# Optimization experiments

Measured on AMD Instinct MI355X. Metric: run time of the kernel, lower is better.

The kernel has to match this reference:

```python
import jax, jax.numpy as jnp
import numpy as np

MEMORY_SIZE = 2000
SHAPE = (512, 8, 8)
D = int(np.prod(SHAPE))  # 32768
LAM = 0.0005  # hard-shrink threshold (1/memory_size convention)
EPS = 1e-12   # F.normalize eps


def _l2_normalize(x, axis):
    # matches F.normalize(p=2): x / max(||x||, eps)
    n = jnp.sqrt(jnp.sum(x * x, axis=axis, keepdims=True))
    return x / jnp.maximum(n, EPS)


def _hard_shrink(x):
    return jnp.where(jnp.abs(x) > LAM, x, jnp.zeros_like(x))


def setup_inputs() -> dict:
    key = jax.random.key(0)
    k1, k2 = jax.random.split(key)
    feature = jax.random.normal(k1, (256, *SHAPE), dtype=jnp.float32)
    memory = jax.random.normal(k2, (MEMORY_SIZE, D), dtype=jnp.float32)
    return {"feature": feature, "memory": memory}


def reference(feature, memory):
    B = feature.shape[0]
    flat = feature.reshape(B, -1)                     # [B, D]
    fn = _l2_normalize(flat, axis=1)                  # [B, D]
    mn = _l2_normalize(memory, axis=1)                # [M, D]
    w = jnp.einsum('bd,md->bm', fn, mn)               # cosine similarity [B, M]
    w = jax.nn.softmax(w, axis=1)
    w = _hard_shrink(w)
    w = jax.nn.softmax(w, axis=1)
    mem_feat = jnp.einsum('bm,md->bd', w, memory)     # [B, D]
    mem_feat = mem_feat.reshape(B, *SHAPE)
    return (mem_feat, w)
```

## Files before the change

### kernel.cpp

```cpp
#include <hip/hip_runtime.h>
#include <math.h>


#define D_DIM 32768
#define B_DIM 256
#define M_DIM 2000
#define M_PAD 2048
#define NS1 16
#define KSLAB (D_DIM / NS1)
#define LAM 0.0005f
#define LDB 72

typedef __attribute__((ext_vector_type(8))) short bf16x8;
typedef __attribute__((ext_vector_type(4))) float f32x4;

#define GLOBAL_AS __attribute__((address_space(1)))
#define LDS_AS __attribute__((address_space(3)))

__device__ __forceinline__ void cp_async16(const void* g, void* l) {
  __builtin_amdgcn_global_load_lds((const GLOBAL_AS unsigned int*)g,
                                   (LDS_AS unsigned int*)l, 16, 0, 0);
}

__device__ __forceinline__ unsigned short f2bf(float f) {
  union { float f; unsigned u; } v; v.f = f;
  unsigned r = v.u + 0x7FFFu + ((v.u >> 16) & 1u);
  return (unsigned short)(r >> 16);
}

__global__ __launch_bounds__(256) void zero_kernel(float* __restrict__ p, int n) {
  int i = blockIdx.x * 256 + threadIdx.x;
  if (i < n) p[i] = 0.f;
}

__global__ __launch_bounds__(256) void prep_feat_kernel(const float* __restrict__ src,
                                                        unsigned short* __restrict__ dst,
                                                        float* __restrict__ rn_inv) {
  const size_t row = blockIdx.x;
  const int t = threadIdx.x;
  const float4* p = (const float4*)(src + row * (size_t)D_DIM);
  ushort4* q = (ushort4*)(dst + row * (size_t)D_DIM);
  float s = 0.f;
  for (int i = t; i < D_DIM / 4; i += 256) {
    float4 v = p[i];
    s = fmaf(v.x, v.x, s); s = fmaf(v.y, v.y, s);
    s = fmaf(v.z, v.z, s); s = fmaf(v.w, v.w, s);
    ushort4 b; b.x = f2bf(v.x); b.y = f2bf(v.y); b.z = f2bf(v.z); b.w = f2bf(v.w);
    q[i] = b;
  }
  #pragma unroll
  for (int off = 32; off > 0; off >>= 1) s += __shfl_down(s, off, 64);
  __shared__ float partial[4];
  if ((t & 63) == 0) partial[t >> 6] = s;
  __syncthreads();
  if (t == 0) {
    float tt = partial[0] + partial[1] + partial[2] + partial[3];
    rn_inv[row] = 1.0f / fmaxf(sqrtf(tt), 1e-12f);
  }
}

__global__ __launch_bounds__(256) void gemm1_fused(const unsigned short* __restrict__ F16,
                                                   const float* __restrict__ mem,
                                                   unsigned short* __restrict__ Mem16,
                                                   float* __restrict__ Spart,
                                                   float* __restrict__ rnm_sq) {
  __shared__ __align__(16) unsigned short Asm[256 * 64];
  __shared__ __align__(16) unsigned short Bsm[64 * LDB];
  const int t = threadIdx.x;
  const int m0 = blockIdx.x * 64;
  const int kbase = blockIdx.y * KSLAB;
  const int wid = t >> 6, lane = t & 63;
  const int lr = lane & 15, kq = lane >> 4;
  const int l8 = lane & 7, lrow = lane >> 3;

  const int brow = t >> 2;
  const int bcol = (t & 3) * 16;
  const int gm = m0 + brow;
  const bool bvalid = gm < M_DIM;
  const float* Bg = mem + (size_t)gm * D_DIM + kbase + bcol;
  unsigned short* M16g = Mem16 + (size_t)gm * D_DIM + kbase + bcol;

  const unsigned short* Ab = F16 + (size_t)(64 * wid + lrow) * D_DIM + kbase + (l8 ^ lrow) * 8;

  f32x4 acc[4][4] = {};
  float ss = 0.f;

  for (int kt = 0; kt < KSLAB / 64; kt++) {
    const int kk = kt * 64;
    __syncthreads();
    #pragma unroll
    for (int i = 0; i < 8; i++)
      cp_async16(Ab + kk + (size_t)(8 * i) * D_DIM, &Asm[(64 * wid + 8 * i) * 64]);

    float4 v[4];
    #pragma unroll
    for (int j = 0; j < 4; j++)
      v[j] = bvalid ? *(const float4*)(Bg + kk + 4 * j) : make_float4(0.f, 0.f, 0.f, 0.f);
    ushort4 c[4];
    #pragma unroll
    for (int j = 0; j < 4; j++) {
      ss = fmaf(v[j].x, v[j].x, ss); ss = fmaf(v[j].y, v[j].y, ss);
      ss = fmaf(v[j].z, v[j].z, ss); ss = fmaf(v[j].w, v[j].w, ss);
      c[j].x = f2bf(v[j].x); c[j].y = f2bf(v[j].y);
      c[j].z = f2bf(v[j].z); c[j].w = f2bf(v[j].w);
    }
    *(ushort4*)&Bsm[brow * LDB + bcol + 0]  = c[0];
    *(ushort4*)&Bsm[brow * LDB + bcol + 4]  = c[1];
    *(ushort4*)&Bsm[brow * LDB + bcol + 8]  = c[2];
    *(ushort4*)&Bsm[brow * LDB + bcol + 12] = c[3];
    *(ushort4*)(M16g + kk + 0)  = c[0];
    *(ushort4*)(M16g + kk + 4)  = c[1];
    *(ushort4*)(M16g + kk + 8)  = c[2];
    *(ushort4*)(M16g + kk + 12) = c[3];
    __syncthreads();

    bf16x8 bfr[2][4];
    #pragma unroll
    for (int h = 0; h < 2; h++)
      #pragma unroll
      for (int ni = 0; ni < 4; ni++)
        bfr[h][ni] = *(const bf16x8*)&Bsm[(ni * 16 + lr) * LDB + h * 32 + kq * 8];
    #pragma unroll
    for (int mi = 0; mi < 4; mi++) {
      #pragma unroll
      for (int h = 0; h < 2; h++) {
        const int sw = ((h * 4 + kq) ^ (lr & 7)) * 8;
        const bf16x8 af = *(const bf16x8*)&Asm[(wid * 64 + mi * 16 + lr) * 64 + sw];
        #pragma unroll
        for (int ni = 0; ni < 4; ni++)
          acc[mi][ni] = __builtin_amdgcn_mfma_f32_16x16x32_bf16(af, bfr[h][ni], acc[mi][ni], 0, 0, 0);
      }
    }
  }

  ss += __shfl_down(ss, 2, 4);
  ss += __shfl_down(ss, 1, 4);
  if ((t & 3) == 0 && bvalid) atomicAdd(&rnm_sq[gm], ss);

  float* Sp = Spart + (size_t)blockIdx.y * (B_DIM * M_PAD);
  #pragma unroll
  for (int mi = 0; mi < 4; mi++) {
    const int b0 = wid * 64 + mi * 16 + kq * 4;
    #pragma unroll
    for (int ni = 0; ni < 4; ni++) {
      const int col = m0 + ni * 16 + lr;
      #pragma unroll
      for (int j = 0; j < 4; j++)
        Sp[(size_t)(b0 + j) * M_PAD + col] = acc[mi][ni][j];
    }
  }
}

__device__ __forceinline__ float block_reduce(float x, bool is_max, float* red,
                                              int wid, int lane) {
  #pragma unroll
  for (int off = 32; off > 0; off >>= 1) {
    float o = __shfl_down(x, off, 64);
    x = is_max ? fmaxf(x, o) : (x + o);
  }
  __syncthreads();
  if (lane == 0) red[wid] = x;
  __syncthreads();
  return is_max ? fmaxf(fmaxf(red[0], red[1]), fmaxf(red[2], red[3]))
                : (red[0] + red[1] + red[2] + red[3]);
}

__global__ __launch_bounds__(256) void softmax_kernel(const float* __restrict__ Spart,
                                                      const float* __restrict__ rnf,
                                                      const float* __restrict__ rnm_sq,
                                                      float* __restrict__ wout,
                                                      unsigned short* __restrict__ wbf) {
  const int b = blockIdx.x;
  const int t = threadIdx.x;
  const int wid = t >> 6, lane = t & 63;
  const float sf = rnf[b];
  __shared__ float red[4];

  float v[8];
  #pragma unroll
  for (int i = 0; i < 8; i++) {
    const int m = t + 256 * i;
    float a = 0.f;
    #pragma unroll
    for (int s = 0; s < NS1; s++)
      a += Spart[(size_t)s * (B_DIM * M_PAD) + (size_t)b * M_PAD + m];
    const float mscale = 1.0f / fmaxf(sqrtf(rnm_sq[m]), 1e-12f);
    v[i] = (m < M_DIM) ? a * (sf * mscale) : -INFINITY;
  }
  float mx = v[0];
  #pragma unroll
  for (int i = 1; i < 8; i++) mx = fmaxf(mx, v[i]);
  mx = block_reduce(mx, true, red, wid, lane);

  float e[8]; float sum = 0.f;
  #pragma unroll
  for (int i = 0; i < 8; i++) { e[i] = expf(v[i] - mx); sum += e[i]; }
  sum = block_reduce(sum, false, red, wid, lane);
  const float inv = 1.f / sum;

  float s2[8];
  #pragma unroll
  for (int i = 0; i < 8; i++) {
    float w1 = e[i] * inv;
    s2[i] = (w1 > LAM) ? w1 : 0.f;
  }
  float mx2 = 0.f;
  #pragma unroll
  for (int i = 0; i < 8; i++) mx2 = fmaxf(mx2, s2[i]);
  mx2 = block_reduce(mx2, true, red, wid, lane);

  float e2[8]; float sum2 = 0.f;
  #pragma unroll
  for (int i = 0; i < 8; i++) {
    const int m = t + 256 * i;
    e2[i] = (m < M_DIM) ? expf(s2[i] - mx2) : 0.f;
    sum2 += e2[i];
  }
  sum2 = block_reduce(sum2, false, red, wid, lane);
  const float inv2 = 1.f / sum2;

  #pragma unroll
  for (int i = 0; i < 8; i++) {
    const int m = t + 256 * i;
    const float w2 = e2[i] * inv2;
    if (m < M_DIM) wout[(size_t)b * M_DIM + m] = w2;
    wbf[(size_t)b * M_PAD + m] = f2bf(w2);
  }
}

__global__ __launch_bounds__(256) void gemm2_kernel(const unsigned short* __restrict__ W,
                                                    const unsigned short* __restrict__ Bm,
                                                    float* __restrict__ C) {
  __shared__ __align__(16) unsigned short Wsm[256 * 64];
  __shared__ __align__(16) unsigned short Bt[64 * LDB];
  const int t = threadIdx.x;
  const int n0 = blockIdx.x * 64;
  const int wid = t >> 6, lane = t & 63;
  const int lr = lane & 15, kq = lane >> 4;
  const int l8 = lane & 7, lrow = lane >> 3;

  const unsigned short* Wb = W + (size_t)(64 * wid + lrow) * M_PAD + (l8 ^ lrow) * 8;

  const int kl2 = 2 * (t >> 4);
  const int d4 = (t & 15) * 4;

  f32x4 acc[4][4] = {};

  for (int k0 = 0; k0 < M_PAD; k0 += 64) {
    __syncthreads();
    #pragma unroll
    for (int i = 0; i < 8; i++)
      cp_async16(Wb + k0 + (size_t)(8 * i) * M_PAD, &Wsm[(64 * wid + 8 * i) * 64]);
    #pragma unroll
    for (int it = 0; it < 2; it++) {
      const int kl = kl2 + 32 * it;
      const ushort4 va = *(const ushort4*)(Bm + (size_t)(k0 + kl) * D_DIM + n0 + d4);
      const ushort4 vb = *(const ushort4*)(Bm + (size_t)(k0 + kl + 1) * D_DIM + n0 + d4);
      const unsigned p0 = (unsigned)va.x | ((unsigned)vb.x << 16);
      const unsigned p1 = (unsigned)va.y | ((unsigned)vb.y << 16);
      const unsigned p2 = (unsigned)va.z | ((unsigned)vb.z << 16);
      const unsigned p3 = (unsigned)va.w | ((unsigned)vb.w << 16);
      *(unsigned*)&Bt[(d4 + 0) * LDB + kl] = p0;
      *(unsigned*)&Bt[(d4 + 1) * LDB + kl] = p1;
      *(unsigned*)&Bt[(d4 + 2) * LDB + kl] = p2;
      *(unsigned*)&Bt[(d4 + 3) * LDB + kl] = p3;
    }
    __syncthreads();

    bf16x8 bfr[2][4];
    #pragma unroll
    for (int h = 0; h < 2; h++)
      #pragma unroll
      for (int ni = 0; ni < 4; ni++)
        bfr[h][ni] = *(const bf16x8*)&Bt[(ni * 16 + lr) * LDB + h * 32 + kq * 8];
    #pragma unroll
    for (int mi = 0; mi < 4; mi++) {
      #pragma unroll
      for (int h = 0; h < 2; h++) {
        const int sw = ((h * 4 + kq) ^ (lr & 7)) * 8;
        const bf16x8 af = *(const bf16x8*)&Wsm[(wid * 64 + mi * 16 + lr) * 64 + sw];
        #pragma unroll
        for (int ni = 0; ni < 4; ni++)
          acc[mi][ni] = __builtin_amdgcn_mfma_f32_16x16x32_bf16(af, bfr[h][ni], acc[mi][ni], 0, 0, 0);
      }
    }
  }
  #pragma unroll
  for (int mi = 0; mi < 4; mi++) {
    const int b0 = wid * 64 + mi * 16 + kq * 4;
    #pragma unroll
    for (int ni = 0; ni < 4; ni++) {
      const int col = n0 + ni * 16 + lr;
      #pragma unroll
      for (int j = 0; j < 4; j++)
        C[(size_t)(b0 + j) * D_DIM + col] = acc[mi][ni][j];
    }
  }
}

extern "C" void kernel_launch(void* const* d_in, const int* in_sizes, int n_in,
                              void* d_out, int out_size, void* d_ws, size_t ws_size,
                              hipStream_t stream) {
  const float* feature = (const float*)d_in[0];
  const float* memory  = (const float*)d_in[1];
  float* out_feat = (float*)d_out;
  float* out_w = out_feat + (size_t)B_DIM * D_DIM;

  char* ws = (char*)d_ws;
  unsigned short* Mem16 = (unsigned short*)ws;
  unsigned short* F16   = (unsigned short*)(ws + 134217728ull);
  unsigned short* Wbf   = (unsigned short*)(ws + 150994944ull);
  float* Spart          = (float*)(ws + 152043520ull);
  float* rnm_sq         = (float*)(ws + 185597952ull);
  float* rnf            = (float*)(ws + 185606144ull);

  zero_kernel<<<(M_PAD + 255) / 256, 256, 0, stream>>>(rnm_sq, M_PAD);
  prep_feat_kernel<<<B_DIM, 256, 0, stream>>>(feature, F16, rnf);
  gemm1_fused<<<dim3(M_PAD / 64, NS1), 256, 0, stream>>>(F16, memory, Mem16, Spart, rnm_sq);
  softmax_kernel<<<B_DIM, 256, 0, stream>>>(Spart, rnf, rnm_sq, out_w, Wbf);
  gemm2_kernel<<<D_DIM / 64, 256, 0, stream>>>(Wbf, Mem16, out_feat);
}
```

Before: 519.9 us.

## Drop bf16 memory copy; convert fp32 memory on the fly in gemm2

gemm1 no longer writes a bf16 copy of the memory matrix to workspace. gemm2 now reads the fp32 memory directly, converts it to bf16 and stores it into a swizzled LDS tile. This removes a large global write plus its later read, but gemm2 must now read twice as many bytes using scalar strided loads. The change also vectorizes the Spart reads and weight writes in the softmax, and adds an occupancy hint of 3 blocks to both GEMM launch bounds.

Measured after the change: 497.1 us. -4.4%, faster.

```diff
diff --git a/kernel.cpp b/kernel.cpp
--- a/kernel.cpp
+++ b/kernel.cpp
@@ -59,11 +59,10 @@
   }
 }
 
-__global__ __launch_bounds__(256) void gemm1_fused(const unsigned short* __restrict__ F16,
-                                                   const float* __restrict__ mem,
-                                                   unsigned short* __restrict__ Mem16,
-                                                   float* __restrict__ Spart,
-                                                   float* __restrict__ rnm_sq) {
+__global__ __launch_bounds__(256, 3) void gemm1_fused(const unsigned short* __restrict__ F16,
+                                                      const float* __restrict__ mem,
+                                                      float* __restrict__ Spart,
+                                                      float* __restrict__ rnm_sq) {
   __shared__ __align__(16) unsigned short Asm[256 * 64];
   __shared__ __align__(16) unsigned short Bsm[64 * LDB];
   const int t = threadIdx.x;
@@ -78,7 +77,6 @@
   const int gm = m0 + brow;
   const bool bvalid = gm < M_DIM;
   const float* Bg = mem + (size_t)gm * D_DIM + kbase + bcol;
-  unsigned short* M16g = Mem16 + (size_t)gm * D_DIM + kbase + bcol;
 
   const unsigned short* Ab = F16 + (size_t)(64 * wid + lrow) * D_DIM + kbase + (l8 ^ lrow) * 8;
 
@@ -96,22 +94,14 @@
     #pragma unroll
     for (int j = 0; j < 4; j++)
       v[j] = bvalid ? *(const float4*)(Bg + kk + 4 * j) : make_float4(0.f, 0.f, 0.f, 0.f);
-    ushort4 c[4];
     #pragma unroll
     for (int j = 0; j < 4; j++) {
       ss = fmaf(v[j].x, v[j].x, ss); ss = fmaf(v[j].y, v[j].y, ss);
       ss = fmaf(v[j].z, v[j].z, ss); ss = fmaf(v[j].w, v[j].w, ss);
-      c[j].x = f2bf(v[j].x); c[j].y = f2bf(v[j].y);
-      c[j].z = f2bf(v[j].z); c[j].w = f2bf(v[j].w);
-    }
-    *(ushort4*)&Bsm[brow * LDB + bcol + 0]  = c[0];
-    *(ushort4*)&Bsm[brow * LDB + bcol + 4]  = c[1];
-    *(ushort4*)&Bsm[brow * LDB + bcol + 8]  = c[2];
-    *(ushort4*)&Bsm[brow * LDB + bcol + 12] = c[3];
-    *(ushort4*)(M16g + kk + 0)  = c[0];
-    *(ushort4*)(M16g + kk + 4)  = c[1];
-    *(ushort4*)(M16g + kk + 8)  = c[2];
-    *(ushort4*)(M16g + kk + 12) = c[3];
+      ushort4 c; c.x = f2bf(v[j].x); c.y = f2bf(v[j].y);
+      c.z = f2bf(v[j].z); c.w = f2bf(v[j].w);
+      *(ushort4*)&Bsm[brow * LDB + bcol + 4 * j] = c;
+    }
     __syncthreads();
 
     bf16x8 bfr[2][4];
@@ -178,14 +168,18 @@
 
   float v[8];
   #pragma unroll
-  for (int i = 0; i < 8; i++) {
-    const int m = t + 256 * i;
-    float a = 0.f;
+  for (int g = 0; g < 2; g++) {
+    const int mq = g * 1024 + 4 * t;
+    f32x4 a = {0.f, 0.f, 0.f, 0.f};
     #pragma unroll
     for (int s = 0; s < NS1; s++)
-      a += Spart[(size_t)s * (B_DIM * M_PAD) + (size_t)b * M_PAD + m];
-    const float mscale = 1.0f / fmaxf(sqrtf(rnm_sq[m]), 1e-12f);
-    v[i] = (m < M_DIM) ? a * (sf * mscale) : -INFINITY;
+      a += *(const f32x4*)&Spart[(size_t)s * (B_DIM * M_PAD) + (size_t)b * M_PAD + mq];
+    #pragma unroll
+    for (int j = 0; j < 4; j++) {
+      const int m = mq + j;
+      const float msc = 1.0f / fmaxf(sqrtf(rnm_sq[m]), 1e-12f);
+      v[g * 4 + j] = (m < M_DIM) ? a[j] * (sf * msc) : -INFINITY;
+    }
   }
   float mx = v[0];
   #pragma unroll
@@ -211,28 +205,38 @@
 
   float e2[8]; float sum2 = 0.f;
   #pragma unroll
-  for (int i = 0; i < 8; i++) {
-    const int m = t + 256 * i;
-    e2[i] = (m < M_DIM) ? expf(s2[i] - mx2) : 0.f;
-    sum2 += e2[i];
-  }
+  for (int g = 0; g < 2; g++)
+    #pragma unroll
+    for (int j = 0; j < 4; j++) {
+      const int i = g * 4 + j;
+      const int m = g * 1024 + 4 * t + j;
+      e2[i] = (m < M_DIM) ? expf(s2[i] - mx2) : 0.f;
+      sum2 += e2[i];
+    }
   sum2 = block_reduce(sum2, false, red, wid, lane);
   const float inv2 = 1.f / sum2;
 
   #pragma unroll
-  for (int i = 0; i < 8; i++) {
-    const int m = t + 256 * i;
-    const float w2 = e2[i] * inv2;
-    if (m < M_DIM) wout[(size_t)b * M_DIM + m] = w2;
-    wbf[(size_t)b * M_PAD + m] = f2bf(w2);
-  }
-}
-
-__global__ __launch_bounds__(256) void gemm2_kernel(const unsigned short* __restrict__ W,
-                                                    const unsigned short* __restrict__ Bm,
-                                                    float* __restrict__ C) {
+  for (int g = 0; g < 2; g++) {
+    const int mq = g * 1024 + 4 * t;
+    float4 wq; ushort4 bq;
+    float* wp = (float*)&wq;
+    #pragma unroll
+    for (int j = 0; j < 4; j++) {
+      const float w2 = e2[g * 4 + j] * inv2;
+      wp[j] = w2;
+      ((unsigned short*)&bq)[j] = f2bf(w2);
+    }
+    if (mq + 3 < M_DIM) *(float4*)&wout[(size_t)b * M_DIM + mq] = wq;
+    *(ushort4*)&wbf[(size_t)b * M_PAD + mq] = bq;
+  }
+}
+
+__global__ __launch_bounds__(256, 3) void gemm2_kernel(const unsigned short* __restrict__ W,
+                                                       const float* __restrict__ mem,
+                                                       float* __restrict__ C) {
   __shared__ __align__(16) unsigned short Wsm[256 * 64];
-  __shared__ __align__(16) unsigned short Bt[64 * LDB];
+  __shared__ __align__(16) unsigned short Bt[64 * 64];
   const int t = threadIdx.x;
   const int n0 = blockIdx.x * 64;
   const int wid = t >> 6, lane = t & 63;
@@ -241,8 +245,9 @@
 
   const unsigned short* Wb = W + (size_t)(64 * wid + lrow) * M_PAD + (l8 ^ lrow) * 8;
 
-  const int kl2 = 2 * (t >> 4);
-  const int d4 = (t & 15) * 4;
+  const int bn = t & 63;
+  const int kc = t >> 6;
+  const float* Bg = mem + (size_t)(kc * 16) * D_DIM + n0 + bn;
 
   f32x4 acc[4][4] = {};
 
@@ -251,20 +256,22 @@
     #pragma unroll
     for (int i = 0; i < 8; i++)
       cp_async16(Wb + k0 + (size_t)(8 * i) * M_PAD, &Wsm[(64 * wid + 8 * i) * 64]);
-    #pragma unroll
-    for (int it = 0; it < 2; it++) {
-      const int kl = kl2 + 32 * it;
-      const ushort4 va = *(const ushort4*)(Bm + (size_t)(k0 + kl) * D_DIM + n0 + d4);
-      const ushort4 vb = *(const ushort4*)(Bm + (size_t)(k0 + kl + 1) * D_DIM + n0 + d4);
-      const unsigned p0 = (unsigned)va.x | ((unsigned)vb.x << 16);
-      const unsigned p1 = (unsigned)va.y | ((unsigned)vb.y << 16);
-      const unsigned p2 = (unsigned)va.z | ((unsigned)vb.z << 16);
-      const unsigned p3 = (unsigned)va.w | ((unsigned)vb.w << 16);
-      *(unsigned*)&Bt[(d4 + 0) * LDB + kl] = p0;
-      *(unsigned*)&Bt[(d4 + 1) * LDB + kl] = p1;
-      *(unsigned*)&Bt[(d4 + 2) * LDB + kl] = p2;
-      *(unsigned*)&Bt[(d4 + 3) * LDB + kl] = p3;
-    }
+
+    bf16x8 kb0, kb1;
+    #pragma unroll
+    for (int j = 0; j < 8; j++) {
+      const int k = k0 + kc * 16 + j;
+      const float f = (k < M_DIM) ? Bg[(size_t)(k0 + j) * D_DIM] : 0.f;
+      kb0[j] = (short)f2bf(f);
+    }
+    #pragma unroll
+    for (int j = 8; j < 16; j++) {
+      const int k = k0 + kc * 16 + j;
+      const float f = (k < M_DIM) ? Bg[(size_t)(k0 + j) * D_DIM] : 0.f;
+      kb1[j - 8] = (short)f2bf(f);
+    }
+    *(bf16x8*)&Bt[bn * 64 + (((kc * 2 + 0) ^ (bn & 7)) * 8)] = kb0;
+    *(bf16x8*)&Bt[bn * 64 + (((kc * 2 + 1) ^ (bn & 7)) * 8)] = kb1;
     __syncthreads();
 
     bf16x8 bfr[2][4];
@@ -272,7 +279,7 @@
     for (int h = 0; h < 2; h++)
       #pragma unroll
       for (int ni = 0; ni < 4; ni++)
-        bfr[h][ni] = *(const bf16x8*)&Bt[(ni * 16 + lr) * LDB + h * 32 + kq * 8];
+        bfr[h][ni] = *(const bf16x8*)&Bt[(ni * 16 + lr) * 64 + (((h * 4 + kq) ^ (lr & 7)) * 8)];
     #pragma unroll
     for (int mi = 0; mi < 4; mi++) {
       #pragma unroll
@@ -307,16 +314,15 @@
   float* out_w = out_feat + (size_t)B_DIM * D_DIM;
 
   char* ws = (char*)d_ws;
-  unsigned short* Mem16 = (unsigned short*)ws;
-  unsigned short* F16   = (unsigned short*)(ws + 134217728ull);
-  unsigned short* Wbf   = (unsigned short*)(ws + 150994944ull);
-  float* Spart          = (float*)(ws + 152043520ull);
-  float* rnm_sq         = (float*)(ws + 185597952ull);
-  float* rnf            = (float*)(ws + 185606144ull);
+  unsigned short* F16 = (unsigned short*)ws;
+  float* Spart        = (float*)(ws + 16777216ull);
+  unsigned short* Wbf = (unsigned short*)(ws + 50331648ull);
+  float* rnm_sq       = (float*)(ws + 51380224ull);
+  float* rnf          = (float*)(ws + 51388416ull);
 
   zero_kernel<<<(M_PAD + 255) / 256, 256, 0, stream>>>(rnm_sq, M_PAD);
   prep_feat_kernel<<<B_DIM, 256, 0, stream>>>(feature, F16, rnf);
-  gemm1_fused<<<dim3(M_PAD / 64, NS1), 256, 0, stream>>>(F16, memory, Mem16, Spart, rnm_sq);
+  gemm1_fused<<<dim3(M_PAD / 64, NS1), 256, 0, stream>>>(F16, memory, Spart, rnm_sq);
   softmax_kernel<<<B_DIM, 256, 0, stream>>>(Spart, rnf, rnm_sq, out_w, Wbf);
-  gemm2_kernel<<<D_DIM / 64, 256, 0, stream>>>(Wbf, Mem16, out_feat);
-}
+  gemm2_kernel<<<D_DIM / 64, 256, 0, stream>>>(Wbf, memory, out_feat);
+}
```
